# Kernel tuning notes

Hardware: AMD Instinct MI355X
Metric: run time of the kernel (lower is better)

Reference implementation:

```python
import jax, jax.numpy as jnp
import numpy as np

B, D, T = 16, 64, 3000
N_CB, K = 8, 1024


def setup_inputs() -> dict:
    key = jax.random.key(0)
    k1, k2 = jax.random.split(key)
    x = jax.random.normal(k1, (B, D, T), dtype=jnp.float32)
    embeds = jax.random.normal(k2, (N_CB, K, D), dtype=jnp.float32) * 0.02
    return {"x": x, "embeds": embeds}


def _vq_stage(r_flat, embed):
    """One VectorQuantize layer on flattened [N, D] input (eval mode).

    Returns (quantized_st [N,D], indices [N], commit+codebook loss, utilization).
    """
    # squared Euclidean distances [N, K]; argmin is identical to cdist argmin
    d2 = (jnp.sum(r_flat * r_flat, axis=-1, keepdims=True)
          - 2.0 * (r_flat @ embed.T)
          + jnp.sum(embed * embed, axis=-1))
    idx = jnp.argmin(d2, axis=-1)                      # [N]
    q = embed[idx]                                     # [N, D] gather
    sg = jax.lax.stop_gradient
    commit = jnp.mean((r_flat - sg(q)) ** 2)
    codebook = jnp.mean((q - sg(r_flat)) ** 2)
    q_st = r_flat + sg(q - r_flat)                     # straight-through
    used = jnp.zeros((K,), dtype=jnp.float32).at[idx].set(1.0)
    util = jnp.sum(used) / K                           # == len(unique)/K
    return q_st, idx, commit + codebook, util


def reference(x, embeds):
    """ResidualVQ forward (eval mode): x [B, D, T], embeds [n_cb, K, D]."""
    sg = jax.lax.stop_gradient
    residual = x
    quantized_total = jnp.zeros_like(x)
    all_indices = []
    total_commit = jnp.float32(0.0)
    total_util = jnp.float32(0.0)
    for i in range(N_CB):
        r_flat = residual.transpose(0, 2, 1).reshape(-1, D)  # [B*T, D]
        q_st_flat, idx, commit, util = _vq_stage(r_flat, embeds[i])
        q_st = q_st_flat.reshape(x.shape[0], x.shape[2], D).transpose(0, 2, 1)
        residual = residual - sg(q_st)
        quantized_total = quantized_total + q_st
        all_indices.append(idx)
        total_commit = total_commit + commit
        total_util = total_util + util
    indices = jnp.stack(all_indices, axis=0)           # [n_cb, B*T]
    return quantized_total, indices, total_commit / N_CB, total_util / N_CB
```

## Files before the change

kernel.cpp:

```cpp
#include <hip/hip_runtime.h>
#include <hip/hip_bf16.h>
#include <math.h>

#define Bn   16
#define Dn   64
#define Tn   3000
#define Nn   (Bn*Tn)
#define NCB  8
#define Kn   1024
#define KTB  64
#define NCHK (Kn/KTB)
#define NTB  64
#define NBLK (Nn/NTB)
#define QMAX 512

#define SM_RH    0
#define SM_RL    8192
#define SM_RF    16384
#define SM_SESTG 32768
#define SM_SR    36864
#define SM_BEST  37120
#define SM_QCNT  37632
#define SM_QUE   37648
#define SM_BK    39696
#define SM_TOT   39952

#define WS_EHI   12288000
#define WS_SE    13336576
#define WS_USED  13369344
#define WS_LOSS  13402112
#define WS_SEMAX 13402128

#define OUT_QT_OFF  0
#define OUT_IDX_OFF 3072000
#define OUT_SC_OFF  3456000

typedef __attribute__((ext_vector_type(4))) float f32x4;
typedef __attribute__((ext_vector_type(8))) short s16x8;

__device__ __forceinline__ unsigned short f2bf(float x) {
    unsigned int u = __float_as_uint(x);
    unsigned int r = (u + 0x7FFFu + ((u >> 16) & 1u)) >> 16;
    return (unsigned short)r;
}
__device__ __forceinline__ float bf2f(unsigned short h) {
    return __uint_as_float(((unsigned int)h) << 16);
}

__global__ void vq_se(const float* __restrict__ emb, float* __restrict__ se,
                      float* __restrict__ semax)
{
    int r = blockIdx.x * 256 + threadIdx.x;
    if (r < NCB*Kn) {
        const float* p = emb + r*Dn;
        float a0=0.f, a1=0.f, a2=0.f, a3=0.f;
        #pragma unroll
        for (int d = 0; d < Dn; d += 4) {
            a0 = fmaf(p[d+0], p[d+0], a0);
            a1 = fmaf(p[d+1], p[d+1], a1);
            a2 = fmaf(p[d+2], p[d+2], a2);
            a3 = fmaf(p[d+3], p[d+3], a3);
        }
        float v = (a0+a1)+(a2+a3);
        se[r] = v;
        atomicMax((int*)&semax[r >> 10], __float_as_int(v));
    }
}

__global__ void vq_ebf(const float* __restrict__ emb, char* __restrict__ ehi)
{
    int idx = blockIdx.x * 256 + threadIdx.x;
    int r = idx >> 3;
    int sdim = idx & 7;
    const float* p = emb + (size_t)r*Dn + sdim*8;
    s16x8 hh;
    #pragma unroll
    for (int j = 0; j < 8; ++j) hh[j] = (short)f2bf(p[j]);
    int cb = r >> 10, kk = r & 1023, c = kk >> 6, kl = kk & 63;
    int i = kl >> 4, lrow = kl & 15, ks = sdim >> 2, lhi = sdim & 3;
    size_t off = (size_t)cb*131072 + (size_t)c*8192
               + (size_t)((i*2 + ks)*16 + lrow)*64 + lhi*16;
    *(s16x8*)(ehi + off) = hh;
}

__device__ __forceinline__
float vq_rescore(const float* rf, float sr, float sek,
                 const float* __restrict__ emb_cb, int n, int kg)
{
    const float4* ep = (const float4*)(emb_cb + (size_t)kg*Dn);
    float q0=0.f,q1=0.f,q2=0.f,q3=0.f;
    #pragma unroll 4
    for (int m = 0; m < 16; ++m) {
        float4 e4 = ep[m];
        q0 = fmaf(rf[(4*m+0)*64 + n], e4.x, q0);
        q1 = fmaf(rf[(4*m+1)*64 + n], e4.y, q1);
        q2 = fmaf(rf[(4*m+2)*64 + n], e4.z, q2);
        q3 = fmaf(rf[(4*m+3)*64 + n], e4.w, q3);
    }
    float dot = (q0+q1)+(q2+q3);
    return (sr - 2.0f*dot) + sek;
}

__global__ __launch_bounds__(256, 3)
void vq_mega(const float* __restrict__ x, const float* __restrict__ emb,
             const char* __restrict__ ehib, const float* __restrict__ se_g,
             const float* __restrict__ semax_g,
             float* __restrict__ out_qt, float* __restrict__ out_idx,
             float* __restrict__ used_g, float* __restrict__ loss_acc)
{
    __shared__ __align__(16) char smem[SM_TOT];
    float*  rf     = (float*)(smem + SM_RF);
    float*  sestg  = (float*)(smem + SM_SESTG);
    float*  lds_sr = (float*)(smem + SM_SR);
    unsigned long long* best64 = (unsigned long long*)(smem + SM_BEST);
    int*    qcnt   = (int*)(smem + SM_QCNT);
    unsigned int* que = (unsigned int*)(smem + SM_QUE);
    float*  srpart = (float*)(smem + SM_QUE);
    int*    bkL    = (int*)(smem + SM_BK);

    const int tid = threadIdx.x;
    const int n0 = blockIdx.x * NTB;
    const int lane = tid & 63, w = tid >> 6;
    const int lrow = lane & 15, lhi = lane >> 4;
    const int nl = tid & 63;
    const int dg = tid >> 6;
    const int laneoff = lrow*64 + lhi*16;

    {
        const int n = n0 + nl;
        const int b = n / Tn, t = n % Tn;
        const float* gp = x + b*(Dn*Tn) + t;
        float v[16];
        #pragma unroll
        for (int j = 0; j < 16; ++j) v[j] = gp[(dg*16 + j)*Tn];
        float a0=0.f,a1=0.f,a2=0.f,a3=0.f;
        #pragma unroll
        for (int j = 0; j < 16; j += 4) {
            a0 = fmaf(v[j+0], v[j+0], a0);
            a1 = fmaf(v[j+1], v[j+1], a1);
            a2 = fmaf(v[j+2], v[j+2], a2);
            a3 = fmaf(v[j+3], v[j+3], a3);
        }
        srpart[dg*64 + nl] = (a0+a1)+(a2+a3);
        unsigned short hi[16], lo[16];
        #pragma unroll
        for (int j = 0; j < 16; ++j) {
            rf[(dg*16 + j)*64 + nl] = v[j];
            hi[j] = f2bf(v[j]);
            lo[j] = f2bf(v[j] - bf2f(hi[j]));
        }
        s16x8 ph0, ph1, pl0, pl1;
        #pragma unroll
        for (int j = 0; j < 8; ++j) {
            ph0[j] = (short)hi[j];   ph1[j] = (short)hi[j+8];
            pl0[j] = (short)lo[j];   pl1[j] = (short)lo[j+8];
        }
        const int s0 = dg*2, s1 = dg*2 + 1, nx = nl & 7;
        *(s16x8*)(smem + SM_RH + nl*128 + ((s0 ^ nx) << 4)) = ph0;
        *(s16x8*)(smem + SM_RH + nl*128 + ((s1 ^ nx) << 4)) = ph1;
        *(s16x8*)(smem + SM_RL + nl*128 + ((s0 ^ nx) << 4)) = pl0;
        *(s16x8*)(smem + SM_RL + nl*128 + ((s1 ^ nx) << 4)) = pl1;
    }
    if (tid < 64) best64[tid] = ~0ULL;
    if (tid == 0) qcnt[0] = 0;
    __syncthreads();
    if (tid < 64)
        lds_sr[tid] = (srpart[tid] + srpart[64+tid]) + (srpart[128+tid] + srpart[192+tid]);
    *(float4*)&sestg[tid*4] = *(const float4*)&se_g[tid*4];
    __syncthreads();

    float lsum = 0.f;
    const int nlocal = w*16 + lrow;

    for (int s = 0; s < NCB; ++s) {
        const float* emb_s = emb + (size_t)s*(Kn*Dn);
        const char*  eh_s  = ehib + (size_t)s*131072;
        const float semx = semax_g[s];
        const float band = 0.0095f * sqrtf(semx * lds_sr[nlocal]) + 2e-4f;
        float m_run = INFINITY;

        for (int c = 0; c < NCHK; ++c) {
            const char* ec = eh_s + ((size_t)c << 13);
            s16x8 ahf[2][4];
            #pragma unroll
            for (int ks = 0; ks < 2; ++ks)
                #pragma unroll
                for (int i = 0; i < 4; ++i)
                    ahf[ks][i] = *(const s16x8*)(ec + (((i<<1) + ks) << 10) + laneoff);

            f32x4 acc[4];
            #pragma unroll
            for (int i = 0; i < 4; ++i) acc[i] = (f32x4){0.f,0.f,0.f,0.f};
            #pragma unroll
            for (int ks = 0; ks < 2; ++ks) {
                const int sdim = ks*4 + lhi;
                const int swz = ((sdim ^ (lrow & 7)) << 4);
                const size_t roff = (size_t)(w*16 + lrow)*128 + swz;
                s16x8 bh = *(const s16x8*)(smem + SM_RH + roff);
                s16x8 bl = *(const s16x8*)(smem + SM_RL + roff);
                #pragma unroll
                for (int i = 0; i < 4; ++i) {
                    acc[i] = __builtin_amdgcn_mfma_f32_16x16x32_bf16(ahf[ks][i], bh, acc[i], 0, 0, 0);
                    acc[i] = __builtin_amdgcn_mfma_f32_16x16x32_bf16(ahf[ks][i], bl, acc[i], 0, 0, 0);
                }
            }

            float mi[4];
            float m = INFINITY;
            #pragma unroll
            for (int i = 0; i < 4; ++i) {
                f32x4 se4 = *(const f32x4*)&sestg[c*64 + i*16 + lhi*4];
                #pragma unroll
                for (int rg = 0; rg < 4; ++rg)
                    acc[i][rg] = se4[rg] - 2.0f*acc[i][rg];
                float a = fminf(fminf(acc[i][0], acc[i][1]), fminf(acc[i][2], acc[i][3]));
                mi[i] = a;
                m = fminf(m, a);
            }
            m = fminf(m, __shfl_xor(m, 16, 64));
            m = fminf(m, __shfl_xor(m, 32, 64));
            const float thr = fminf(m_run, m) + band;
            m_run = fminf(m_run, m);

            #pragma unroll
            for (int i = 0; i < 4; ++i) {
                if (__any(mi[i] <= thr)) {
                    #pragma unroll
                    for (int rg = 0; rg < 4; ++rg) {
                        if (acc[i][rg] <= thr) {
                            int kl = i*16 + lhi*4 + rg;
                            int kg = c*KTB + kl;
                            int slot = atomicAdd(qcnt, 1);
                            if (slot < QMAX) {
                                que[slot] = ((unsigned)nlocal << 10) | (unsigned)kg;
                            } else {
                                float d2e = vq_rescore(rf, lds_sr[nlocal], sestg[kg],
                                                       emb_s, nlocal, kg);
                                unsigned long long pk =
                                    ((unsigned long long)__float_as_uint(d2e) << 32) | (unsigned)kg;
                                atomicMin(&best64[nlocal], pk);
                            }
                        }
                    }
                }
            }
        }
        __syncthreads();

        const int cnt = min(qcnt[0], QMAX);
        for (int e = tid; e < cnt; e += 256) {
            unsigned ent = que[e];
            int nn = (int)(ent >> 10);
            int kg = (int)(ent & 1023);
            float d2e = vq_rescore(rf, lds_sr[nn], sestg[kg], emb_s, nn, kg);
            unsigned long long pk =
                ((unsigned long long)__float_as_uint(d2e) << 32) | (unsigned)kg;
            atomicMin(&best64[nn], pk);
        }
        __syncthreads();

        if (tid < 64) {
            int bk = (int)(best64[tid] & 0xFFFFFFFFull) & (Kn - 1);
            bkL[tid] = bk;
            out_idx[s*Nn + n0 + tid] = (float)bk;
            used_g[s*Kn + bk] = 1.0f;
            best64[tid] = ~0ULL;
        }
        if (tid == 0) qcnt[0] = 0;
        __syncthreads();

        const float* ep = emb_s + (size_t)bkL[nl]*Dn;
        if (s < NCB-1) {
            float nv[16];
            #pragma unroll
            for (int j = 0; j < 16; ++j) {
                int d = dg*16 + j;
                float rv = rf[d*64 + nl];
                float q  = ep[d];
                float diff = rv - q;
                lsum = fmaf(diff, diff, lsum);
                float qst = rv + (q - rv);
                nv[j] = rv - qst;
                rf[d*64 + nl] = nv[j];
            }
            float a0=0.f,a1=0.f,a2=0.f,a3=0.f;
            #pragma unroll
            for (int j = 0; j < 16; j += 4) {
                a0 = fmaf(nv[j+0], nv[j+0], a0);
                a1 = fmaf(nv[j+1], nv[j+1], a1);
                a2 = fmaf(nv[j+2], nv[j+2], a2);
                a3 = fmaf(nv[j+3], nv[j+3], a3);
            }
            srpart[dg*64 + nl] = (a0+a1)+(a2+a3);
            unsigned short hi[16], lo[16];
            #pragma unroll
            for (int j = 0; j < 16; ++j) {
                hi[j] = f2bf(nv[j]);
                lo[j] = f2bf(nv[j] - bf2f(hi[j]));
            }
            s16x8 ph0, ph1, pl0, pl1;
            #pragma unroll
            for (int j = 0; j < 8; ++j) {
                ph0[j] = (short)hi[j];   ph1[j] = (short)hi[j+8];
                pl0[j] = (short)lo[j];   pl1[j] = (short)lo[j+8];
            }
            const int s0 = dg*2, s1 = dg*2 + 1, nx = nl & 7;
            *(s16x8*)(smem + SM_RH + nl*128 + ((s0 ^ nx) << 4)) = ph0;
            *(s16x8*)(smem + SM_RH + nl*128 + ((s1 ^ nx) << 4)) = ph1;
            *(s16x8*)(smem + SM_RL + nl*128 + ((s0 ^ nx) << 4)) = pl0;
            *(s16x8*)(smem + SM_RL + nl*128 + ((s1 ^ nx) << 4)) = pl1;
            __syncthreads();
            if (tid < 64)
                lds_sr[tid] = (srpart[tid] + srpart[64+tid])
                            + (srpart[128+tid] + srpart[192+tid]);
            *(float4*)&sestg[tid*4] = *(const float4*)&se_g[(s+1)*Kn + tid*4];
            __syncthreads();
        } else {
            const int n = n0 + nl;
            const int b = n / Tn, t = n % Tn;
            const float* xp = x + b*(Dn*Tn) + t;
            float* qp = out_qt + b*(Dn*Tn) + t;
            #pragma unroll
            for (int j = 0; j < 16; ++j) {
                int d = dg*16 + j;
                float rv = rf[d*64 + nl];
                float q  = ep[d];
                float diff = rv - q;
                lsum = fmaf(diff, diff, lsum);
                float qst = rv + (q - rv);
                float rn = rv - qst;
                qp[d*Tn] = xp[d*Tn] - rn;
            }
        }
    }

    float* red = (float*)(smem + SM_QUE);
    red[tid] = lsum;
    __syncthreads();
    for (int s2 = 128; s2 > 0; s2 >>= 1) {
        if (tid < s2) red[tid] += red[tid + s2];
        __syncthreads();
    }
    if (tid == 0) atomicAdd(loss_acc, red[0]);
}

__global__ void vq_scalars(const float* __restrict__ used, const float* __restrict__ loss_acc,
                           float* __restrict__ out)
{
    __shared__ float red[256];
    float s = 0.f;
    for (int j = threadIdx.x; j < NCB*Kn; j += 256) s += used[j];
    red[threadIdx.x] = s;
    __syncthreads();
    for (int st = 128; st > 0; st >>= 1) {
        if (threadIdx.x < st) red[threadIdx.x] += red[threadIdx.x + st];
        __syncthreads();
    }
    if (threadIdx.x == 0) {
        float sumsq = loss_acc[0];
        float total_loss = 2.0f * sumsq / (float)(Nn*Dn);
        out[OUT_SC_OFF + 0] = total_loss / (float)NCB;
        out[OUT_SC_OFF + 1] = red[0] / (float)(NCB*Kn);
    }
}

extern "C" void kernel_launch(void* const* d_in, const int* in_sizes, int n_in,
                              void* d_out, int out_size, void* d_ws, size_t ws_size,
                              hipStream_t stream)
{
    const float* x      = (const float*)d_in[0];
    const float* embeds = (const float*)d_in[1];
    float* out = (float*)d_out;
    char* ws = (char*)d_ws;

    char*  ehi   = ws + WS_EHI;
    float* se    = (float*)(ws + WS_SE);
    float* used  = (float*)(ws + WS_USED);
    float* loss  = (float*)(ws + WS_LOSS);
    float* semax = (float*)(ws + WS_SEMAX);

    hipMemsetAsync(used, 0, (size_t)NCB*Kn*sizeof(float) + 48, stream);

    vq_se<<<(NCB*Kn + 255)/256, 256, 0, stream>>>(embeds, se, semax);
    vq_ebf<<<256, 256, 0, stream>>>(embeds, ehi);

    vq_mega<<<NBLK, 256, 0, stream>>>(x, embeds, ehi, se, semax,
                                      out + OUT_QT_OFF, out + OUT_IDX_OFF,
                                      used, loss);

    vq_scalars<<<1, 256, 0, stream>>>(used, loss, out);
}
```

Before: 385.8 us.

## Drop low-bf16 residual split, widen rescore band, prefetch codebook chunks

```diff
diff --git a/kernel.cpp b/kernel.cpp
--- a/kernel.cpp
+++ b/kernel.cpp
@@ -12,18 +12,17 @@
 #define NCHK (Kn/KTB)
 #define NTB  64
 #define NBLK (Nn/NTB)
-#define QMAX 512
+#define QMAX 1024
 
 #define SM_RH    0
-#define SM_RL    8192
-#define SM_RF    16384
-#define SM_SESTG 32768
-#define SM_SR    36864
-#define SM_BEST  37120
-#define SM_QCNT  37632
-#define SM_QUE   37648
-#define SM_BK    39696
-#define SM_TOT   39952
+#define SM_RF    8192
+#define SM_SESTG 24576
+#define SM_SR    28672
+#define SM_BEST  28928
+#define SM_QCNT  29440
+#define SM_QUE   29456
+#define SM_BK    33552
+#define SM_TOT   33808
 
 #define WS_EHI   12288000
 #define WS_SE    13336576
@@ -42,9 +41,6 @@
     unsigned int u = __float_as_uint(x);
     unsigned int r = (u + 0x7FFFu + ((u >> 16) & 1u)) >> 16;
     return (unsigned short)r;
-}
-__device__ __forceinline__ float bf2f(unsigned short h) {
-    return __uint_as_float(((unsigned int)h) << 16);
 }
 
 __global__ void vq_se(const float* __restrict__ emb, float* __restrict__ se,
@@ -142,24 +138,20 @@
             a3 = fmaf(v[j+3], v[j+3], a3);
         }
         srpart[dg*64 + nl] = (a0+a1)+(a2+a3);
-        unsigned short hi[16], lo[16];
+        unsigned short hi[16];
         #pragma unroll
         for (int j = 0; j < 16; ++j) {
             rf[(dg*16 + j)*64 + nl] = v[j];
             hi[j] = f2bf(v[j]);
-            lo[j] = f2bf(v[j] - bf2f(hi[j]));
-        }
-        s16x8 ph0, ph1, pl0, pl1;
+        }
+        s16x8 ph0, ph1;
         #pragma unroll
         for (int j = 0; j < 8; ++j) {
             ph0[j] = (short)hi[j];   ph1[j] = (short)hi[j+8];
-            pl0[j] = (short)lo[j];   pl1[j] = (short)lo[j+8];
         }
         const int s0 = dg*2, s1 = dg*2 + 1, nx = nl & 7;
         *(s16x8*)(smem + SM_RH + nl*128 + ((s0 ^ nx) << 4)) = ph0;
         *(s16x8*)(smem + SM_RH + nl*128 + ((s1 ^ nx) << 4)) = ph1;
-        *(s16x8*)(smem + SM_RL + nl*128 + ((s0 ^ nx) << 4)) = pl0;
-        *(s16x8*)(smem + SM_RL + nl*128 + ((s1 ^ nx) << 4)) = pl1;
     }
     if (tid < 64) best64[tid] = ~0ULL;
     if (tid == 0) qcnt[0] = 0;
@@ -176,18 +168,25 @@
         const float* emb_s = emb + (size_t)s*(Kn*Dn);
         const char*  eh_s  = ehib + (size_t)s*131072;
         const float semx = semax_g[s];
-        const float band = 0.0095f * sqrtf(semx * lds_sr[nlocal]) + 2e-4f;
+        const float band = 0.019f * sqrtf(semx * lds_sr[nlocal]) + 2e-4f;
         float m_run = INFINITY;
 
-        for (int c = 0; c < NCHK; ++c) {
-            const char* ec = eh_s + ((size_t)c << 13);
-            s16x8 ahf[2][4];
-            #pragma unroll
-            for (int ks = 0; ks < 2; ++ks)
+        s16x8 bufA[2][4], bufB[2][4];
+        #pragma unroll
+        for (int ks = 0; ks < 2; ++ks)
+            #pragma unroll
+            for (int i = 0; i < 4; ++i)
+                bufA[ks][i] = *(const s16x8*)(eh_s + (((i<<1)+ks) << 10) + laneoff);
+
+        auto chunk_body = [&](int c, s16x8 (&cur)[2][4], s16x8 (&nxt)[2][4], bool pre) {
+            if (pre) {
+                const char* en = eh_s + ((size_t)(c+1) << 13);
                 #pragma unroll
-                for (int i = 0; i < 4; ++i)
-                    ahf[ks][i] = *(const s16x8*)(ec + (((i<<1) + ks) << 10) + laneoff);
-
+                for (int ks = 0; ks < 2; ++ks)
+                    #pragma unroll
+                    for (int i = 0; i < 4; ++i)
+                        nxt[ks][i] = *(const s16x8*)(en + (((i<<1)+ks) << 10) + laneoff);
+            }
             f32x4 acc[4];
             #pragma unroll
             for (int i = 0; i < 4; ++i) acc[i] = (f32x4){0.f,0.f,0.f,0.f};
@@ -197,12 +196,9 @@
                 const int swz = ((sdim ^ (lrow & 7)) << 4);
                 const size_t roff = (size_t)(w*16 + lrow)*128 + swz;
                 s16x8 bh = *(const s16x8*)(smem + SM_RH + roff);
-                s16x8 bl = *(const s16x8*)(smem + SM_RL + roff);
                 #pragma unroll
-                for (int i = 0; i < 4; ++i) {
-                    acc[i] = __builtin_amdgcn_mfma_f32_16x16x32_bf16(ahf[ks][i], bh, acc[i], 0, 0, 0);
-                    acc[i] = __builtin_amdgcn_mfma_f32_16x16x32_bf16(ahf[ks][i], bl, acc[i], 0, 0, 0);
-                }
+                for (int i = 0; i < 4; ++i)
+                    acc[i] = __builtin_amdgcn_mfma_f32_16x16x32_bf16(cur[ks][i], bh, acc[i], 0, 0, 0);
             }
 
             float mi[4];
@@ -244,6 +240,11 @@
                     }
                 }
             }
+        };
+
+        for (int cc = 0; cc < NCHK; cc += 2) {
+            chunk_body(cc,     bufA, bufB, true);
+            chunk_body(cc + 1, bufB, bufA, (cc + 2) < NCHK);
         }
         __syncthreads();
 
@@ -292,23 +293,15 @@
                 a3 = fmaf(nv[j+3], nv[j+3], a3);
             }
             srpart[dg*64 + nl] = (a0+a1)+(a2+a3);
-            unsigned short hi[16], lo[16];
-            #pragma unroll
-            for (int j = 0; j < 16; ++j) {
-                hi[j] = f2bf(nv[j]);
-                lo[j] = f2bf(nv[j] - bf2f(hi[j]));
-            }
-            s16x8 ph0, ph1, pl0, pl1;
+            s16x8 ph0, ph1;
             #pragma unroll
             for (int j = 0; j < 8; ++j) {
-                ph0[j] = (short)hi[j];   ph1[j] = (short)hi[j+8];
-                pl0[j] = (short)lo[j];   pl1[j] = (short)lo[j+8];
+                ph0[j] = (short)f2bf(nv[j]);
+                ph1[j] = (short)f2bf(nv[j+8]);
             }
             const int s0 = dg*2, s1 = dg*2 + 1, nx = nl & 7;
             *(s16x8*)(smem + SM_RH + nl*128 + ((s0 ^ nx) << 4)) = ph0;
             *(s16x8*)(smem + SM_RH + nl*128 + ((s1 ^ nx) << 4)) = ph1;
-            *(s16x8*)(smem + SM_RL + nl*128 + ((s0 ^ nx) << 4)) = pl0;
-            *(s16x8*)(smem + SM_RL + nl*128 + ((s1 ^ nx) << 4)) = pl1;
             __syncthreads();
             if (tid < 64)
                 lds_sr[tid] = (srpart[tid] + srpart[64+tid])
```

Result: slower. 728.6 us (+88.8%).
